# Kernel optimization log

Hardware: AMD Instinct MI355X
Metric: run time of the kernel (lower is better)

Reference implementation:

```python
import jax, jax.numpy as jnp
import numpy as np

EMB = 64      # embedding_dim
HID = 128     # hidden_dim
SCALE = 4.0   # InputEmbedding scale
N_TRACKS = 32768


def lstm_cell(x, h, c, W_ih, W_hh, b_ih, b_hh):
    # torch.nn.LSTMCell gate order: i, f, g, o
    gates = x @ W_ih.T + b_ih + h @ W_hh.T + b_hh  # [N, 4*HID]
    i, f, g, o = jnp.split(gates, 4, axis=-1)
    i = jax.nn.sigmoid(i)
    f = jax.nn.sigmoid(f)
    g = jnp.tanh(g)
    o = jax.nn.sigmoid(o)
    c_new = f * c + i * g
    h_new = o * jnp.tanh(c_new)
    return h_new, c_new


def setup_inputs() -> dict:
    key = jax.random.key(0)
    ks = jax.random.split(key, 14)

    def init(k, shape, fan_in):
        b = 1.0 / np.sqrt(fan_in)
        return jax.random.uniform(k, shape, jnp.float32, -b, b)

    return {
        "observed": jax.random.normal(ks[0], (9, N_TRACKS, 2), jnp.float32),
        "prediction": jax.random.normal(ks[1], (12, N_TRACKS, 2), jnp.float32),
        # InputEmbedding: Linear(2, EMB-2) followed by ReLU, 2 tag dims appended
        "W_emb": init(ks[2], (EMB - 2, 2), 2),
        "b_emb": init(ks[3], (EMB - 2,), 2),
        # LSTMCell(EMB, HID)
        "W_ih": init(ks[4], (4 * HID, EMB), HID),
        "W_hh": init(ks[5], (4 * HID, HID), HID),
        "b_ih": init(ks[6], (4 * HID,), HID),
        "b_hh": init(ks[7], (4 * HID,), HID),
        # real_classifier MLP: 128 -> 64 -> 32 -> 1, ReLU after each Linear
        "W1": init(ks[8], (HID // 2, HID), HID),
        "b1": init(ks[9], (HID // 2,), HID),
        "W2": init(ks[10], (HID // 4, HID // 2), HID // 2),
        "b2": init(ks[11], (HID // 4,), HID // 2),
        "W3": init(ks[12], (1, HID // 4), HID // 4),
        "b3": init(ks[13], (1,), HID // 4),
    }


def reference(observed, prediction, W_emb, b_emb, W_ih, W_hh, b_ih, b_hh,
              W1, b1, W2, b2, W3, b3):
    seq = jnp.concatenate([observed, prediction], axis=0)  # [T, N, 2]
    N = seq.shape[1]
    h = jnp.zeros((N, HID), seq.dtype)
    c = jnp.zeros((N, HID), seq.dtype)

    # tag_step: start_enc tag is one-hot at position EMB-2
    tag = jnp.zeros((N, EMB), seq.dtype).at[:, EMB - 2].set(1.0)
    h, c = lstm_cell(tag, h, c, W_ih, W_hh, b_ih, b_hh)

    def step(carry, xs):
        h, c = carry
        obs1, obs2 = xs
        # track visible iff both frames are non-NaN
        mask = ~(jnp.isnan(obs1[:, 0]) | jnp.isnan(obs2[:, 0]))  # [N]
        vel = jnp.where(mask[:, None], obs2 - obs1, 0.0)
        emb = jax.nn.relu((vel * SCALE) @ W_emb.T + b_emb)       # [N, EMB-2]
        emb = jnp.concatenate([emb, jnp.zeros((N, 2), emb.dtype)], axis=1)
        h_new, c_new = lstm_cell(emb, h, c, W_ih, W_hh, b_ih, b_hh)
        # scatter updated states back only for visible tracks
        h = jnp.where(mask[:, None], h_new, h)
        c = jnp.where(mask[:, None], c_new, c)
        return (h, c), None

    (h, c), _ = jax.lax.scan(step, (h, c), (seq[:-1], seq[1:]))

    # real_classifier applied to hidden state of track 0
    x = jax.nn.relu(h[0] @ W1.T + b1)
    x = jax.nn.relu(x @ W2.T + b2)
    scores = jax.nn.relu(x @ W3.T + b3)  # shape (1,)
    return scores
```

## Files before the change

kernel.cpp:

```cpp
#include <hip/hip_runtime.h>
#include <math.h>

#define NT 32768
#define SCALEF 4.0f

__device__ __forceinline__ float rl(float v, int l) {
    return __int_as_float(__builtin_amdgcn_readlane(__float_as_int(v), l));
}

__device__ __forceinline__ void pin(float4 &v) {
    asm volatile("" : "+v"(v.x), "+v"(v.y), "+v"(v.z), "+v"(v.w));
}

__device__ __forceinline__ float sigf(float x) {
    return __builtin_amdgcn_rcpf(1.0f + __expf(-x));
}
__device__ __forceinline__ float tanhfast(float x) {
    return 1.0f - 2.0f * __builtin_amdgcn_rcpf(1.0f + __expf(2.0f * x));
}

__device__ __forceinline__ float frame_val(const float* __restrict__ obs,
                                           const float* __restrict__ pred,
                                           int F, int d) {
    return (F < 9) ? obs[F * (NT * 2) + d] : pred[(F - 9) * (NT * 2) + d];
}

#define MAC4(acc, hv, l, W)                       \
    acc = fmaf(rl(hv, (l) + 0), W.x, acc);        \
    acc = fmaf(rl(hv, (l) + 1), W.y, acc);        \
    acc = fmaf(rl(hv, (l) + 2), W.z, acc);        \
    acc = fmaf(rl(hv, (l) + 3), W.w, acc);

__launch_bounds__(1024, 4)
__global__ void lstm_disc_kernel(const float* __restrict__ observed,
                                 const float* __restrict__ prediction,
                                 const float* __restrict__ W_emb,
                                 const float* __restrict__ b_emb,
                                 const float* __restrict__ W_ih,
                                 const float* __restrict__ W_hh,
                                 const float* __restrict__ b_ih,
                                 const float* __restrict__ b_hh,
                                 const float* __restrict__ W1,
                                 const float* __restrict__ b1,
                                 const float* __restrict__ W2,
                                 const float* __restrict__ b2,
                                 const float* __restrict__ W3,
                                 const float* __restrict__ b3,
                                 float* __restrict__ out)
{
    const int tid  = (int)threadIdx.x;
    const int lane = tid & 63;
    const int j    = tid & 511;
    const int p    = tid >> 9;

    __shared__ float xs[21][64];
    __shared__ float gxh[2][21 * 512];
    __shared__ float ppart[1024];
    __shared__ float hbuf[128];
    __shared__ float velx[21], vely[21], maskf[21];
    __shared__ float mlp1[64];
    __shared__ float mlp2[32];

    const float4* Wi = reinterpret_cast<const float4*>(W_ih + j * 64 + 32 * p);
    float4 C0 = Wi[0], C1 = Wi[1], C2 = Wi[2], C3 = Wi[3];
    float4 C4 = Wi[4], C5 = Wi[5], C6 = Wi[6], C7 = Wi[7];
    const float4* Wh = reinterpret_cast<const float4*>(W_hh + j * 128 + 64 * p);
    float4 D0  = Wh[0],  D1  = Wh[1],  D2  = Wh[2],  D3  = Wh[3];
    float4 D4  = Wh[4],  D5  = Wh[5],  D6  = Wh[6],  D7  = Wh[7];
    float4 D8  = Wh[8],  D9  = Wh[9],  D10 = Wh[10], D11 = Wh[11];
    float4 D12 = Wh[12], D13 = Wh[13], D14 = Wh[14], D15 = Wh[15];
    const float bias = b_ih[j] + b_hh[j];

    if (tid < 20) {
        float ax = frame_val(observed, prediction, tid,     0);
        float ay = frame_val(observed, prediction, tid,     1);
        float bx = frame_val(observed, prediction, tid + 1, 0);
        float by = frame_val(observed, prediction, tid + 1, 1);
        unsigned ua = __float_as_uint(ax) & 0x7fffffffu;
        unsigned ub = __float_as_uint(bx) & 0x7fffffffu;
        bool m = !((ua > 0x7f800000u) || (ub > 0x7f800000u));
        maskf[tid + 1] = m ? 1.0f : 0.0f;
        velx[tid + 1]  = m ? (bx - ax) * SCALEF : 0.0f;
        vely[tid + 1]  = m ? (by - ay) * SCALEF : 0.0f;
    }
    if (tid == 20) { maskf[0] = 1.0f; velx[0] = 0.0f; vely[0] = 0.0f; }
    __syncthreads();

    for (int idx = tid; idx < 21 * 64; idx += 1024) {
        int s = idx >> 6, e = idx & 63;
        float v;
        if (s == 0)       v = (e == 62) ? 1.0f : 0.0f;
        else if (e < 62)  v = fmaxf(velx[s] * W_emb[2 * e] + vely[s] * W_emb[2 * e + 1] + b_emb[e], 0.0f);
        else              v = 0.0f;
        xs[s][e] = v;
    }
    __syncthreads();

    unsigned mbits = 0;
    #pragma unroll
    for (int s = 0; s < 21; ++s) mbits |= (maskf[s] != 0.0f ? 1u : 0u) << s;

    pin(C0); pin(C1); pin(C2); pin(C3); pin(C4); pin(C5); pin(C6); pin(C7);

    float* gmine = &gxh[p][j];
    gmine[0] = (p == 0) ? bias : C7.z;
    const float basev = (p == 0) ? bias : 0.0f;
    float xcs = xs[1][32 * p + (lane & 31)];
    for (int s = 1; s < 21; ++s) {
        float xcn = (s < 20) ? xs[s + 1][32 * p + (lane & 31)] : 0.0f;
        float a0 = basev, a1 = 0.0f;
        MAC4(a0, xcs,  0, C0) MAC4(a1, xcs,  4, C1)
        MAC4(a0, xcs,  8, C2) MAC4(a1, xcs, 12, C3)
        MAC4(a0, xcs, 16, C4) MAC4(a1, xcs, 20, C5)
        MAC4(a0, xcs, 24, C6) MAC4(a1, xcs, 28, C7)
        gmine[s * 512] = a0 + a1;
        xcs = xcn;
    }

    pin(D0);  pin(D1);  pin(D2);  pin(D3);  pin(D4);  pin(D5);  pin(D6);  pin(D7);
    pin(D8);  pin(D9);  pin(D10); pin(D11); pin(D12); pin(D13); pin(D14); pin(D15);

    float hseg = 0.0f;
    float creg = 0.0f;
    for (int s = 0; s < 21; ++s) {
        if (mbits & (1u << s)) {
            float acc0 = gmine[s * 512];
            float acc1 = 0.0f;
            MAC4(acc0, hseg,  0, D0)  MAC4(acc1, hseg,  4, D1)
            MAC4(acc0, hseg,  8, D2)  MAC4(acc1, hseg, 12, D3)
            MAC4(acc0, hseg, 16, D4)  MAC4(acc1, hseg, 20, D5)
            MAC4(acc0, hseg, 24, D6)  MAC4(acc1, hseg, 28, D7)
            MAC4(acc0, hseg, 32, D8)  MAC4(acc1, hseg, 36, D9)
            MAC4(acc0, hseg, 40, D10) MAC4(acc1, hseg, 44, D11)
            MAC4(acc0, hseg, 48, D12) MAC4(acc1, hseg, 52, D13)
            MAC4(acc0, hseg, 56, D14) MAC4(acc1, hseg, 60, D15)
            ppart[tid] = acc0 + acc1;
            __syncthreads();
            if (tid < 128) {
                float gi = sigf(    ppart[tid]       + ppart[512 + tid]);
                float gf = sigf(    ppart[128 + tid] + ppart[640 + tid]);
                float gg = tanhfast(ppart[256 + tid] + ppart[768 + tid]);
                float go = sigf(    ppart[384 + tid] + ppart[896 + tid]);
                creg = fmaf(gf, creg, gi * gg);
                hbuf[tid] = go * tanhfast(creg);
            }
            __syncthreads();
            hseg = hbuf[64 * p + lane];
        }
    }

    if (tid < 64) {
        const float4* W1r = reinterpret_cast<const float4*>(W1 + tid * 128);
        float a = b1[tid];
        #pragma unroll
        for (int q = 0; q < 32; ++q) {
            float4 w = W1r[q];
            a = fmaf(w.x, hbuf[4*q], a);   a = fmaf(w.y, hbuf[4*q+1], a);
            a = fmaf(w.z, hbuf[4*q+2], a); a = fmaf(w.w, hbuf[4*q+3], a);
        }
        mlp1[tid] = fmaxf(a, 0.0f);
    }
    __syncthreads();
    if (tid < 32) {
        const float4* W2r = reinterpret_cast<const float4*>(W2 + tid * 64);
        float a = b2[tid];
        #pragma unroll
        for (int q = 0; q < 16; ++q) {
            float4 w = W2r[q];
            a = fmaf(w.x, mlp1[4*q], a);   a = fmaf(w.y, mlp1[4*q+1], a);
            a = fmaf(w.z, mlp1[4*q+2], a); a = fmaf(w.w, mlp1[4*q+3], a);
        }
        mlp2[tid] = fmaxf(a, 0.0f);
    }
    __syncthreads();
    if (tid == 0) {
        float a = b3[0];
        #pragma unroll
        for (int k = 0; k < 32; ++k) a += W3[k] * mlp2[k];
        out[0] = fmaxf(a, 0.0f);
    }
}

extern "C" void kernel_launch(void* const* d_in, const int* in_sizes, int n_in,
                              void* d_out, int out_size, void* d_ws, size_t ws_size,
                              hipStream_t stream) {
    lstm_disc_kernel<<<1, 1024, 0, stream>>>(
        (const float*)d_in[0],  (const float*)d_in[1],
        (const float*)d_in[2],  (const float*)d_in[3],
        (const float*)d_in[4],  (const float*)d_in[5],
        (const float*)d_in[6],  (const float*)d_in[7],
        (const float*)d_in[8],  (const float*)d_in[9],
        (const float*)d_in[10], (const float*)d_in[11],
        (const float*)d_in[12], (const float*)d_in[13],
        (float*)d_out);
}
```

Before: 121.3 us.

## Pack LSTM weights and states to fp16 and use dot2 with LDS-resident W_hh

Converts W_ih and W_hh to packed fp16 pairs and computes the gate dot products with the fdot2 builtin, halving the readlane broadcasts and multiply-adds. W_hh moves from registers into a swizzled LDS buffer that is prefetched inside the loop. The separate input-projection precompute pass is dropped and the x-projection is fused into each recurrent step. This trades fp32 accuracy for fp16 weights and hidden state, and adds LDS reads to every step.

```diff
diff --git a/kernel.cpp b/kernel.cpp
--- a/kernel.cpp
+++ b/kernel.cpp
@@ -4,12 +4,32 @@
 #define NT 32768
 #define SCALEF 4.0f
 
-__device__ __forceinline__ float rl(float v, int l) {
-    return __int_as_float(__builtin_amdgcn_readlane(__float_as_int(v), l));
-}
-
-__device__ __forceinline__ void pin(float4 &v) {
-    asm volatile("" : "+v"(v.x), "+v"(v.y), "+v"(v.z), "+v"(v.w));
+typedef _Float16 h2v __attribute__((ext_vector_type(2)));
+
+__device__ __forceinline__ unsigned rlu(unsigned u, int l) {
+    return (unsigned)__builtin_amdgcn_readlane((int)u, l);
+}
+
+__device__ __forceinline__ unsigned pk2(float lo, float hi) {
+    unsigned a = (unsigned)__builtin_bit_cast(unsigned short, (_Float16)lo);
+    unsigned b = (unsigned)__builtin_bit_cast(unsigned short, (_Float16)hi);
+    return a | (b << 16);
+}
+__device__ __forceinline__ float upk_lo(unsigned u) {
+    return (float)__builtin_bit_cast(_Float16, (unsigned short)(u & 0xffffu));
+}
+__device__ __forceinline__ float upk_hi(unsigned u) {
+    return (float)__builtin_bit_cast(_Float16, (unsigned short)(u >> 16));
+}
+
+__device__ __forceinline__ float dot2(unsigned w, unsigned h, float acc) {
+#if defined(__has_builtin) && __has_builtin(__builtin_amdgcn_fdot2)
+    return __builtin_amdgcn_fdot2(__builtin_bit_cast(h2v, w),
+                                  __builtin_bit_cast(h2v, h), acc, false);
+#else
+    acc = fmaf(upk_lo(w), upk_lo(h), acc);
+    return fmaf(upk_hi(w), upk_hi(h), acc);
+#endif
 }
 
 __device__ __forceinline__ float sigf(float x) {
@@ -24,12 +44,6 @@
                                            int F, int d) {
     return (F < 9) ? obs[F * (NT * 2) + d] : pred[(F - 9) * (NT * 2) + d];
 }
-
-#define MAC4(acc, hv, l, W)                       \
-    acc = fmaf(rl(hv, (l) + 0), W.x, acc);        \
-    acc = fmaf(rl(hv, (l) + 1), W.y, acc);        \
-    acc = fmaf(rl(hv, (l) + 2), W.z, acc);        \
-    acc = fmaf(rl(hv, (l) + 3), W.w, acc);
 
 __launch_bounds__(1024, 4)
 __global__ void lstm_disc_kernel(const float* __restrict__ observed,
@@ -52,24 +66,16 @@
     const int lane = tid & 63;
     const int j    = tid & 511;
     const int p    = tid >> 9;
-
-    __shared__ float xs[21][64];
-    __shared__ float gxh[2][21 * 512];
-    __shared__ float ppart[1024];
-    __shared__ float hbuf[128];
-    __shared__ float velx[21], vely[21], maskf[21];
-    __shared__ float mlp1[64];
-    __shared__ float mlp2[32];
-
-    const float4* Wi = reinterpret_cast<const float4*>(W_ih + j * 64 + 32 * p);
-    float4 C0 = Wi[0], C1 = Wi[1], C2 = Wi[2], C3 = Wi[3];
-    float4 C4 = Wi[4], C5 = Wi[5], C6 = Wi[6], C7 = Wi[7];
-    const float4* Wh = reinterpret_cast<const float4*>(W_hh + j * 128 + 64 * p);
-    float4 D0  = Wh[0],  D1  = Wh[1],  D2  = Wh[2],  D3  = Wh[3];
-    float4 D4  = Wh[4],  D5  = Wh[5],  D6  = Wh[6],  D7  = Wh[7];
-    float4 D8  = Wh[8],  D9  = Wh[9],  D10 = Wh[10], D11 = Wh[11];
-    float4 D12 = Wh[12], D13 = Wh[13], D14 = Wh[14], D15 = Wh[15];
-    const float bias = b_ih[j] + b_hh[j];
+    const int s7   = tid & 7;
+    const int gbase = tid * 8;
+
+    __shared__ uint4    whh4[1024 * 8];
+    __shared__ unsigned xs_pk[21 * 32];
+    __shared__ float    ppart[1024];
+    __shared__ unsigned hpk[64];
+    __shared__ float    hfin[128];
+    __shared__ float    velx[21], vely[21], maskf[21];
+    __shared__ float    mlp1[64], mlp2[32];
 
     if (tid < 20) {
         float ax = frame_val(observed, prediction, tid,     0);
@@ -84,68 +90,92 @@
         vely[tid + 1]  = m ? (by - ay) * SCALEF : 0.0f;
     }
     if (tid == 20) { maskf[0] = 1.0f; velx[0] = 0.0f; vely[0] = 0.0f; }
-    __syncthreads();
-
+
+    unsigned xw[16];
+    {
+        const float4* Wi = reinterpret_cast<const float4*>(W_ih + j * 64 + 32 * p);
+        #pragma unroll
+        for (int q = 0; q < 8; ++q) {
+            float4 w = Wi[q];
+            xw[2 * q]     = pk2(w.x, w.y);
+            xw[2 * q + 1] = pk2(w.z, w.w);
+        }
+        #pragma unroll
+        for (int q = 0; q < 16; ++q) asm volatile("" : "+v"(xw[q]));
+    }
+    const float bias = b_ih[j] + b_hh[j];
+
+    __syncthreads();
+
+    unsigned short* xs16 = (unsigned short*)xs_pk;
     for (int idx = tid; idx < 21 * 64; idx += 1024) {
         int s = idx >> 6, e = idx & 63;
         float v;
-        if (s == 0)       v = (e == 62) ? 1.0f : 0.0f;
-        else if (e < 62)  v = fmaxf(velx[s] * W_emb[2 * e] + vely[s] * W_emb[2 * e + 1] + b_emb[e], 0.0f);
-        else              v = 0.0f;
-        xs[s][e] = v;
-    }
-    __syncthreads();
+        if (s == 0)      v = (e == 62) ? 1.0f : 0.0f;
+        else if (e < 62) v = fmaxf(velx[s] * W_emb[2 * e] + vely[s] * W_emb[2 * e + 1] + b_emb[e], 0.0f);
+        else             v = 0.0f;
+        xs16[s * 64 + e] = __builtin_bit_cast(unsigned short, (_Float16)v);
+    }
+
+    {
+        const float4* Wh = reinterpret_cast<const float4*>(W_hh + j * 128 + 64 * p);
+        #pragma unroll
+        for (int g = 0; g < 8; ++g) {
+            float4 wa = Wh[2 * g], wb = Wh[2 * g + 1];
+            uint4 u;
+            u.x = pk2(wa.x, wa.y); u.y = pk2(wa.z, wa.w);
+            u.z = pk2(wb.x, wb.y); u.w = pk2(wb.z, wb.w);
+            whh4[gbase + (g ^ s7)] = u;
+        }
+    }
 
     unsigned mbits = 0;
     #pragma unroll
     for (int s = 0; s < 21; ++s) mbits |= (maskf[s] != 0.0f ? 1u : 0u) << s;
 
-    pin(C0); pin(C1); pin(C2); pin(C3); pin(C4); pin(C5); pin(C6); pin(C7);
-
-    float* gmine = &gxh[p][j];
-    gmine[0] = (p == 0) ? bias : C7.z;
-    const float basev = (p == 0) ? bias : 0.0f;
-    float xcs = xs[1][32 * p + (lane & 31)];
-    for (int s = 1; s < 21; ++s) {
-        float xcn = (s < 20) ? xs[s + 1][32 * p + (lane & 31)] : 0.0f;
-        float a0 = basev, a1 = 0.0f;
-        MAC4(a0, xcs,  0, C0) MAC4(a1, xcs,  4, C1)
-        MAC4(a0, xcs,  8, C2) MAC4(a1, xcs, 12, C3)
-        MAC4(a0, xcs, 16, C4) MAC4(a1, xcs, 20, C5)
-        MAC4(a0, xcs, 24, C6) MAC4(a1, xcs, 28, C7)
-        gmine[s * 512] = a0 + a1;
-        xcs = xcn;
-    }
-
-    pin(D0);  pin(D1);  pin(D2);  pin(D3);  pin(D4);  pin(D5);  pin(D6);  pin(D7);
-    pin(D8);  pin(D9);  pin(D10); pin(D11); pin(D12); pin(D13); pin(D14); pin(D15);
-
-    float hseg = 0.0f;
+    __syncthreads();
+
+    unsigned short* hpk16 = (unsigned short*)hpk;
     float creg = 0.0f;
+    unsigned hp = 0u;
     for (int s = 0; s < 21; ++s) {
         if (mbits & (1u << s)) {
-            float acc0 = gmine[s * 512];
-            float acc1 = 0.0f;
-            MAC4(acc0, hseg,  0, D0)  MAC4(acc1, hseg,  4, D1)
-            MAC4(acc0, hseg,  8, D2)  MAC4(acc1, hseg, 12, D3)
-            MAC4(acc0, hseg, 16, D4)  MAC4(acc1, hseg, 20, D5)
-            MAC4(acc0, hseg, 24, D6)  MAC4(acc1, hseg, 28, D7)
-            MAC4(acc0, hseg, 32, D8)  MAC4(acc1, hseg, 36, D9)
-            MAC4(acc0, hseg, 40, D10) MAC4(acc1, hseg, 44, D11)
-            MAC4(acc0, hseg, 48, D12) MAC4(acc1, hseg, 52, D13)
-            MAC4(acc0, hseg, 56, D14) MAC4(acc1, hseg, 60, D15)
-            ppart[tid] = acc0 + acc1;
+            unsigned xp = xs_pk[s * 32 + 16 * p + (lane & 15)];
+            uint4 wA = whh4[gbase + (0 ^ s7)];
+            uint4 wB = whh4[gbase + (1 ^ s7)];
+            float a0 = (p == 0) ? bias : 0.0f;
+            float a1 = 0.0f;
+            #pragma unroll
+            for (int g = 0; g < 8; ++g) {
+                uint4 wc = (g & 1) ? wB : wA;
+                if (g + 2 < 8) {
+                    uint4 wn = whh4[gbase + ((g + 2) ^ s7)];
+                    if (g & 1) wB = wn; else wA = wn;
+                }
+                a0 = dot2(wc.x, rlu(hp, 4 * g + 0), a0);
+                a1 = dot2(wc.y, rlu(hp, 4 * g + 1), a1);
+                a0 = dot2(wc.z, rlu(hp, 4 * g + 2), a0);
+                a1 = dot2(wc.w, rlu(hp, 4 * g + 3), a1);
+            }
+            #pragma unroll
+            for (int q = 0; q < 16; ++q) {
+                if (q & 1) a1 = dot2(xw[q], rlu(xp, q), a1);
+                else       a0 = dot2(xw[q], rlu(xp, q), a0);
+            }
+            ppart[tid] = a0 + a1;
             __syncthreads();
             if (tid < 128) {
-                float gi = sigf(    ppart[tid]       + ppart[512 + tid]);
+                float gi = sigf(    ppart[tid      ] + ppart[512 + tid]);
                 float gf = sigf(    ppart[128 + tid] + ppart[640 + tid]);
                 float gg = tanhfast(ppart[256 + tid] + ppart[768 + tid]);
                 float go = sigf(    ppart[384 + tid] + ppart[896 + tid]);
                 creg = fmaf(gf, creg, gi * gg);
-                hbuf[tid] = go * tanhfast(creg);
+                float hv = go * tanhfast(creg);
+                hfin[tid] = hv;
+                hpk16[tid] = __builtin_bit_cast(unsigned short, (_Float16)hv);
             }
             __syncthreads();
-            hseg = hbuf[64 * p + lane];
+            hp = hpk[32 * p + (lane & 31)];
         }
     }
 
@@ -155,8 +185,8 @@
         #pragma unroll
         for (int q = 0; q < 32; ++q) {
             float4 w = W1r[q];
-            a = fmaf(w.x, hbuf[4*q], a);   a = fmaf(w.y, hbuf[4*q+1], a);
-            a = fmaf(w.z, hbuf[4*q+2], a); a = fmaf(w.w, hbuf[4*q+3], a);
+            a = fmaf(w.x, hfin[4*q], a);   a = fmaf(w.y, hfin[4*q+1], a);
+            a = fmaf(w.z, hfin[4*q+2], a); a = fmaf(w.w, hfin[4*q+3], a);
         }
         mlp1[tid] = fmaxf(a, 0.0f);
     }
```

After: 113.5 us. 6.4% less time.
